# Performance work log

Measured on AMD Instinct MI355X. Metric: run time of the kernel, lower is better.

The kernel has to match this reference:

```python
import jax, jax.numpy as jnp
import numpy as np

B, S, D_IN, D_OUT = 8, 2048, 1024, 64

def setup_inputs() -> dict:
    key = jax.random.key(0)
    ks = jax.random.split(key, 6)
    return {
        "inputs_for_keys": jax.random.normal(ks[0], (B, S, D_IN), jnp.float32),
        "inputs_for_values": jax.random.normal(ks[1], (B, S, D_IN), jnp.float32),
        "inputs_for_queries": jax.random.normal(ks[2], (B, S, D_IN), jnp.float32),
        "K": jax.random.normal(ks[3], (D_IN, D_OUT), jnp.float32) * (1.0 / np.sqrt(D_IN)),
        "V": jax.random.normal(ks[4], (D_IN, D_OUT), jnp.float32) * (1.0 / np.sqrt(D_IN)),
        "Q": jax.random.normal(ks[5], (D_IN, D_OUT), jnp.float32) * (1.0 / np.sqrt(D_IN)),
    }

def reference(inputs_for_keys, inputs_for_values, inputs_for_queries, K, V, Q):
    # Project to per-head key/value/query spaces: [B, S, D_OUT]
    keys = jnp.einsum('bsd,de->bse', inputs_for_keys, K)
    values = jnp.einsum('bsd,de->bse', inputs_for_values, V)
    queries = jnp.einsum('bsd,de->bse', inputs_for_queries, Q)
    d_k = keys.shape[-1]
    # Scaled dot-product scores: [B, Sq, Sk]
    score = jnp.einsum('bqe,bke->bqk', queries, keys) / jnp.sqrt(jnp.float32(d_k))
    # Causal mask: -inf strictly above the diagonal (query i attends to keys <= i)
    sq, sk = score.shape[1], score.shape[2]
    causal = jnp.triu(jnp.full((sq, sk), -jnp.inf, dtype=score.dtype), k=1)
    score = score + causal[None, :, :]
    weights = jax.nn.softmax(score, axis=-1)
    # Attention output: [B, Sq, D_OUT]
    return jnp.einsum('bqk,bke->bqe', weights, values)
```

## Files before the change

kernel.cpp:

```cpp
#include <hip/hip_runtime.h>
#include <stdint.h>

#define BB   8
#define SS   2048
#define DIN  1024
#define DOUT 64

typedef __bf16 bf16_t;
typedef __bf16 bf16x8 __attribute__((ext_vector_type(8)));
typedef float  f32x4  __attribute__((ext_vector_type(4)));
typedef unsigned int u32x4 __attribute__((ext_vector_type(4)));

#define LOG2E 1.44269504088896f

__global__ void prep_weights(const float* __restrict__ Kw,
                             const float* __restrict__ Vw,
                             const float* __restrict__ Qw,
                             bf16_t* __restrict__ fw) {
    int proj = blockIdx.x >> 4;
    int seg  = blockIdx.x & 15;
    const float* W = (proj == 0) ? Kw : (proj == 1) ? Vw : Qw;
    float scale = (proj == 2) ? 0.125f : 1.0f;
    bf16_t* out = fw + proj * 65536;
    int base = seg * 4096;
#pragma unroll
    for (int i = 0; i < 16; ++i) {
        int idx  = base + i * 256 + threadIdx.x;
        int j    = idx & 7;
        int lane = (idx >> 3) & 63;
        int nt   = (idx >> 9) & 3;
        int kk   = idx >> 11;
        int k    = kk * 32 + (lane >> 4) * 8 + j;
        int col  = nt * 16 + (lane & 15);
        out[idx] = (bf16_t)(W[k * DOUT + col] * scale);
    }
}

__global__ __launch_bounds__(256) void proj_kernel(
    const float* __restrict__ Xk, const float* __restrict__ Xv,
    const float* __restrict__ Xq, const bf16_t* __restrict__ fw,
    bf16_t* __restrict__ outK, bf16_t* __restrict__ outV,
    bf16_t* __restrict__ outQ) {
    __shared__ __align__(16) bf16_t lds[16384];

    int proj = blockIdx.y;
    const float* X  = (proj == 0) ? Xk : (proj == 1) ? Xv : Xq;
    bf16_t* out     = (proj == 0) ? outK : (proj == 1) ? outV : outQ;
    const bf16_t* fwp = fw + proj * 65536;

    int tid  = threadIdx.x;
    int lane = tid & 63;
    int w    = tid >> 6;
    int row0 = blockIdx.x * 64 + w * 16;
    int arow = row0 + (lane & 15);
    const float* aptr = X + (size_t)arow * DIN + ((lane >> 4) * 8);

    f32x4 acc[4];
#pragma unroll
    for (int nt = 0; nt < 4; ++nt) acc[nt] = (f32x4)(0.0f);

    for (int c = 0; c < 4; ++c) {
        __syncthreads();
        const u32x4* src = (const u32x4*)(fwp + c * 16384);
        u32x4* dst = (u32x4*)lds;
#pragma unroll
        for (int i = 0; i < 8; ++i) dst[tid + 256 * i] = src[tid + 256 * i];
        __syncthreads();

#pragma unroll
        for (int kkl = 0; kkl < 8; ++kkl) {
            int kglob = c * 256 + kkl * 32;
            f32x4 a0 = *(const f32x4*)(aptr + kglob);
            f32x4 a1 = *(const f32x4*)(aptr + kglob + 4);
            bf16x8 af;
            af[0] = (bf16_t)a0[0]; af[1] = (bf16_t)a0[1];
            af[2] = (bf16_t)a0[2]; af[3] = (bf16_t)a0[3];
            af[4] = (bf16_t)a1[0]; af[5] = (bf16_t)a1[1];
            af[6] = (bf16_t)a1[2]; af[7] = (bf16_t)a1[3];
#pragma unroll
            for (int nt = 0; nt < 4; ++nt) {
                bf16x8 bfv = *(const bf16x8*)((const char*)lds +
                                ((size_t)((kkl * 4 + nt) * 64 + lane) * 16));
                acc[nt] = __builtin_amdgcn_mfma_f32_16x16x32_bf16(af, bfv, acc[nt], 0, 0, 0);
            }
        }
    }

#pragma unroll
    for (int nt = 0; nt < 4; ++nt) {
#pragma unroll
        for (int r = 0; r < 4; ++r) {
            int row = row0 + (lane >> 4) * 4 + r;
            int col = nt * 16 + (lane & 15);
            out[(size_t)row * DOUT + col] = (bf16_t)acc[nt][r];
        }
    }
}

__global__ __launch_bounds__(256) void attn_kernel(
    const bf16_t* __restrict__ Kp, const bf16_t* __restrict__ Vp,
    const bf16_t* __restrict__ Qp, float* __restrict__ out) {
    __shared__ __align__(16) bf16_t Klds[64 * 64];
    __shared__ __align__(16) bf16_t Vlds[64 * 64];
    __shared__ __align__(16) bf16_t Plds[4][16 * 64];

    int tid   = threadIdx.x;
    int lane  = tid & 63;
    int w     = tid >> 6;
    int qtile = blockIdx.x;
    int batch = blockIdx.y;

    const bf16_t* Kb = Kp + (size_t)batch * SS * DOUT;
    const bf16_t* Vb = Vp + (size_t)batch * SS * DOUT;
    const bf16_t* Qb = Qp + (size_t)batch * SS * DOUT;

    bf16x8 aq[2];
    {
        int r = qtile * 64 + w * 16 + (lane & 15);
        const bf16_t* qp = Qb + (size_t)r * DOUT + (lane >> 4) * 8;
        aq[0] = *(const bf16x8*)(qp);
        aq[1] = *(const bf16x8*)(qp + 32);
    }

    float m[4], lsum[4];
    f32x4 acc[4];
#pragma unroll
    for (int r = 0; r < 4; ++r) { m[r] = -1e30f; lsum[r] = 0.0f; }
#pragma unroll
    for (int nt = 0; nt < 4; ++nt) acc[nt] = (f32x4)(0.0f);

    int ntiles = qtile + 1;
    for (int j = 0; j < ntiles; ++j) {
        __syncthreads();
#pragma unroll
        for (int i = 0; i < 2; ++i) {
            int c   = tid + 256 * i;
            int key = c >> 3;
            int d0  = (c & 7) * 8;
            u32x4 v = *(const u32x4*)(Kb + ((size_t)(j * 64 + key)) * DOUT + d0);
            *(u32x4*)((char*)Klds + key * 128 + ((d0 * 2) ^ ((key & 7) << 4))) = v;
        }
#pragma unroll
        for (int i = 0; i < 2; ++i) {
            int c   = tid + 256 * i;
            int key = c >> 3;
            int d0  = (c & 7) * 8;
            bf16x8 v = *(const bf16x8*)(Vb + ((size_t)(j * 64 + key)) * DOUT + d0);
#pragma unroll
            for (int jj = 0; jj < 8; ++jj) {
                int d = d0 + jj;
                *(bf16_t*)((char*)Vlds + d * 128 + ((key * 2) ^ ((d & 7) << 4))) = v[jj];
            }
        }
        __syncthreads();

        f32x4 sfr[4];
#pragma unroll
        for (int nt = 0; nt < 4; ++nt) sfr[nt] = (f32x4)(0.0f);
#pragma unroll
        for (int kk = 0; kk < 2; ++kk) {
            int d0 = kk * 32 + (lane >> 4) * 8;
#pragma unroll
            for (int nt = 0; nt < 4; ++nt) {
                int key = nt * 16 + (lane & 15);
                bf16x8 bk = *(const bf16x8*)((char*)Klds + key * 128 +
                                             ((d0 * 2) ^ ((key & 7) << 4)));
                sfr[nt] = __builtin_amdgcn_mfma_f32_16x16x32_bf16(aq[kk], bk, sfr[nt], 0, 0, 0);
            }
        }

        if (j == qtile) {
#pragma unroll
            for (int nt = 0; nt < 4; ++nt) {
                int key = nt * 16 + (lane & 15);
#pragma unroll
                for (int r = 0; r < 4; ++r) {
                    int q = w * 16 + (lane >> 4) * 4 + r;
                    if (key > q) sfr[nt][r] = -1e30f;
                }
            }
        }

        float pf[4][4];
#pragma unroll
        for (int r = 0; r < 4; ++r) {
            float mx = fmaxf(fmaxf(sfr[0][r], sfr[1][r]), fmaxf(sfr[2][r], sfr[3][r]));
            mx = fmaxf(mx, __shfl_xor(mx, 1));
            mx = fmaxf(mx, __shfl_xor(mx, 2));
            mx = fmaxf(mx, __shfl_xor(mx, 4));
            mx = fmaxf(mx, __shfl_xor(mx, 8));
            float mn = fmaxf(m[r], mx);
            float scale = exp2f((m[r] - mn) * LOG2E);
            m[r] = mn;
            float rs = 0.0f;
#pragma unroll
            for (int nt = 0; nt < 4; ++nt) {
                float p = exp2f((sfr[nt][r] - mn) * LOG2E);
                pf[nt][r] = p;
                rs += p;
            }
            rs += __shfl_xor(rs, 1);
            rs += __shfl_xor(rs, 2);
            rs += __shfl_xor(rs, 4);
            rs += __shfl_xor(rs, 8);
            lsum[r] = lsum[r] * scale + rs;
#pragma unroll
            for (int nt = 0; nt < 4; ++nt) acc[nt][r] *= scale;
        }

#pragma unroll
        for (int nt = 0; nt < 4; ++nt) {
            int key = nt * 16 + (lane & 15);
#pragma unroll
            for (int r = 0; r < 4; ++r) {
                int q = (lane >> 4) * 4 + r;
                *(bf16_t*)((char*)&Plds[w][0] + q * 128 +
                           ((key * 2) ^ ((q & 7) << 4))) = (bf16_t)pf[nt][r];
            }
        }
        __syncthreads();

#pragma unroll
        for (int kk = 0; kk < 2; ++kk) {
            int k0 = kk * 32 + (lane >> 4) * 8;
            int q  = lane & 15;
            bf16x8 ap = *(const bf16x8*)((char*)&Plds[w][0] + q * 128 +
                                         ((k0 * 2) ^ ((q & 7) << 4)));
#pragma unroll
            for (int nt = 0; nt < 4; ++nt) {
                int d = nt * 16 + (lane & 15);
                bf16x8 bv = *(const bf16x8*)((char*)Vlds + d * 128 +
                                             ((k0 * 2) ^ ((d & 7) << 4)));
                acc[nt] = __builtin_amdgcn_mfma_f32_16x16x32_bf16(ap, bv, acc[nt], 0, 0, 0);
            }
        }
    }

    float* ob = out + ((size_t)batch * SS + qtile * 64 + w * 16) * DOUT;
#pragma unroll
    for (int nt = 0; nt < 4; ++nt) {
#pragma unroll
        for (int r = 0; r < 4; ++r) {
            int q = (lane >> 4) * 4 + r;
            int d = nt * 16 + (lane & 15);
            ob[(size_t)q * DOUT + d] = acc[nt][r] / lsum[r];
        }
    }
}

extern "C" void kernel_launch(void* const* d_in, const int* in_sizes, int n_in,
                              void* d_out, int out_size, void* d_ws, size_t ws_size,
                              hipStream_t stream) {
    const float* Xk = (const float*)d_in[0];
    const float* Xv = (const float*)d_in[1];
    const float* Xq = (const float*)d_in[2];
    const float* Kw = (const float*)d_in[3];
    const float* Vw = (const float*)d_in[4];
    const float* Qw = (const float*)d_in[5];

    bf16_t* Kp = (bf16_t*)d_ws;
    bf16_t* Vp = Kp + (size_t)BB * SS * DOUT;
    bf16_t* Qp = Vp + (size_t)BB * SS * DOUT;
    bf16_t* fw = Qp + (size_t)BB * SS * DOUT;

    prep_weights<<<dim3(48), dim3(256), 0, stream>>>(Kw, Vw, Qw, fw);
    proj_kernel<<<dim3(256, 3), dim3(256), 0, stream>>>(Xk, Xv, Xq, fw, Kp, Vp, Qp);
    attn_kernel<<<dim3(32, 8), dim3(256), 0, stream>>>(Kp, Vp, Qp, (float*)d_out);
}
```

Baseline: 109.5 us.

## Restructure projection kernel as split-K with LDS-staged A and register-streamed weights

The projection kernel now has each block handle 16 rows, so the grid grows from 256 to 1024 blocks per projection. Each block stages its fp32 input rows into swizzled bf16 LDS with coalesced loads. The K dimension is split across the four waves, each reading its weight fragments straight from global memory with a one-step register prefetch, and the partial results are reduced through LDS before being written out. This is meant to raise parallelism and coalescing on the memory-bound input read and to drop the repeated weight-to-LDS staging loops. In exchange it adds an LDS reduction, extra barriers and more global weight traffic per block.

```diff
diff --git a/kernel.cpp b/kernel.cpp
--- a/kernel.cpp
+++ b/kernel.cpp
@@ -7,6 +7,7 @@
 #define DOUT 64
 
 typedef __bf16 bf16_t;
+typedef __bf16 bf16x4 __attribute__((ext_vector_type(4)));
 typedef __bf16 bf16x8 __attribute__((ext_vector_type(8)));
 typedef float  f32x4  __attribute__((ext_vector_type(4)));
 typedef unsigned int u32x4 __attribute__((ext_vector_type(4)));
@@ -36,64 +37,87 @@
     }
 }
 
-__global__ __launch_bounds__(256) void proj_kernel(
+__global__ __launch_bounds__(256, 4) void proj_kernel(
     const float* __restrict__ Xk, const float* __restrict__ Xv,
     const float* __restrict__ Xq, const bf16_t* __restrict__ fw,
     bf16_t* __restrict__ outK, bf16_t* __restrict__ outV,
     bf16_t* __restrict__ outQ) {
-    __shared__ __align__(16) bf16_t lds[16384];
+    __shared__ __align__(128) char Alds[32768];
+
+    int tid  = threadIdx.x;
+    int lane = tid & 63;
+    int w    = tid >> 6;
 
     int proj = blockIdx.y;
     const float* X  = (proj == 0) ? Xk : (proj == 1) ? Xv : Xq;
     bf16_t* out     = (proj == 0) ? outK : (proj == 1) ? outV : outQ;
     const bf16_t* fwp = fw + proj * 65536;
 
-    int tid  = threadIdx.x;
-    int lane = tid & 63;
-    int w    = tid >> 6;
-    int row0 = blockIdx.x * 64 + w * 16;
-    int arow = row0 + (lane & 15);
-    const float* aptr = X + (size_t)arow * DIN + ((lane >> 4) * 8);
+    int row0 = blockIdx.x * 16;
+
+#pragma unroll
+    for (int b = 0; b < 2; ++b) {
+        f32x4 v[8];
+#pragma unroll
+        for (int j = 0; j < 8; ++j)
+            v[j] = *(const f32x4*)(X + (size_t)(row0 + b * 8 + j) * DIN + tid * 4);
+#pragma unroll
+        for (int j = 0; j < 8; ++j) {
+            int row = b * 8 + j;
+            bf16x4 bv;
+            bv[0] = (bf16_t)v[j][0]; bv[1] = (bf16_t)v[j][1];
+            bv[2] = (bf16_t)v[j][2]; bv[3] = (bf16_t)v[j][3];
+            *(bf16x4*)(Alds + row * 2048 + ((tid * 8) ^ ((row & 7) << 4))) = bv;
+        }
+    }
+    __syncthreads();
 
     f32x4 acc[4];
 #pragma unroll
     for (int nt = 0; nt < 4; ++nt) acc[nt] = (f32x4)(0.0f);
 
-    for (int c = 0; c < 4; ++c) {
-        __syncthreads();
-        const u32x4* src = (const u32x4*)(fwp + c * 16384);
-        u32x4* dst = (u32x4*)lds;
-#pragma unroll
-        for (int i = 0; i < 8; ++i) dst[tid + 256 * i] = src[tid + 256 * i];
-        __syncthreads();
-
-#pragma unroll
-        for (int kkl = 0; kkl < 8; ++kkl) {
-            int kglob = c * 256 + kkl * 32;
-            f32x4 a0 = *(const f32x4*)(aptr + kglob);
-            f32x4 a1 = *(const f32x4*)(aptr + kglob + 4);
-            bf16x8 af;
-            af[0] = (bf16_t)a0[0]; af[1] = (bf16_t)a0[1];
-            af[2] = (bf16_t)a0[2]; af[3] = (bf16_t)a0[3];
-            af[4] = (bf16_t)a1[0]; af[5] = (bf16_t)a1[1];
-            af[6] = (bf16_t)a1[2]; af[7] = (bf16_t)a1[3];
-#pragma unroll
-            for (int nt = 0; nt < 4; ++nt) {
-                bf16x8 bfv = *(const bf16x8*)((const char*)lds +
-                                ((size_t)((kkl * 4 + nt) * 64 + lane) * 16));
-                acc[nt] = __builtin_amdgcn_mfma_f32_16x16x32_bf16(af, bfv, acc[nt], 0, 0, 0);
-            }
-        }
-    }
-
-#pragma unroll
-    for (int nt = 0; nt < 4; ++nt) {
+    int arow = lane & 15;
+    const bf16_t* bq = fwp + (size_t)(w * 8) * 2048 + lane * 8;
+
+    bf16x8 bnow[4];
+#pragma unroll
+    for (int nt = 0; nt < 4; ++nt) bnow[nt] = *(const bf16x8*)(bq + nt * 512);
+
+#pragma unroll
+    for (int kkl = 0; kkl < 8; ++kkl) {
+        bf16x8 bnext[4];
+        if (kkl < 7) {
+#pragma unroll
+            for (int nt = 0; nt < 4; ++nt)
+                bnext[nt] = *(const bf16x8*)(bq + (kkl + 1) * 2048 + nt * 512);
+        }
+        int kb = (w * 256 + kkl * 32 + (lane >> 4) * 8) * 2;
+        bf16x8 a = *(const bf16x8*)(Alds + arow * 2048 + (kb ^ ((arow & 7) << 4)));
+#pragma unroll
+        for (int nt = 0; nt < 4; ++nt)
+            acc[nt] = __builtin_amdgcn_mfma_f32_16x16x32_bf16(a, bnow[nt], acc[nt], 0, 0, 0);
+#pragma unroll
+        for (int nt = 0; nt < 4; ++nt) bnow[nt] = bnext[nt];
+    }
+
+    __syncthreads();
+    float* red = (float*)Alds;
+#pragma unroll
+    for (int nt = 0; nt < 4; ++nt)
 #pragma unroll
         for (int r = 0; r < 4; ++r) {
-            int row = row0 + (lane >> 4) * 4 + r;
+            int row = (lane >> 4) * 4 + r;
             int col = nt * 16 + (lane & 15);
-            out[(size_t)row * DOUT + col] = (bf16_t)acc[nt][r];
-        }
+            red[w * 1024 + row * 64 + col] = acc[nt][r];
+        }
+    __syncthreads();
+#pragma unroll
+    for (int i = 0; i < 4; ++i) {
+        int row = (tid >> 6) * 4 + i;
+        int col = tid & 63;
+        float s = red[row * 64 + col] + red[1024 + row * 64 + col] +
+                  red[2048 + row * 64 + col] + red[3072 + row * 64 + col];
+        out[(size_t)(row0 + row) * DOUT + col] = (bf16_t)s;
     }
 }
 
@@ -264,6 +288,6 @@
     bf16_t* fw = Qp + (size_t)BB * SS * DOUT;
 
     prep_weights<<<dim3(48), dim3(256), 0, stream>>>(Kw, Vw, Qw, fw);
-    proj_kernel<<<dim3(256, 3), dim3(256), 0, stream>>>(Xk, Xv, Xq, fw, Kp, Vp, Qp);
+    proj_kernel<<<dim3(1024, 3), dim3(256), 0, stream>>>(Xk, Xv, Xq, fw, Kp, Vp, Qp);
     attn_kernel<<<dim3(32, 8), dim3(256), 0, stream>>>(Kp, Vp, Qp, (float*)d_out);
 }
```

Measured after the change: 113.0 us. 1.03x slower.

## Stage projection tiles through LDS with direct global-to-LDS loads and XOR swizzle

Applied to the files above, without the earlier changes.

The projection kernel is restructured to use 32-row tiles with 1536 blocks. The fp32 activation tile and the bf16 weight slice are streamed into LDS via global_load_lds, in 64-wide K steps, with an XOR swizzle to avoid bank conflicts. Before, each lane loaded activations directly from global memory and whole weight chunks were copied through registers. The aim is better memory-level parallelism and coalescing on the bandwidth-bound 200MB input read, at the cost of more barriers per K step and no double buffering.

```diff
diff --git a/kernel.cpp b/kernel.cpp
--- a/kernel.cpp
+++ b/kernel.cpp
@@ -7,11 +7,18 @@
 #define DOUT 64
 
 typedef __bf16 bf16_t;
+typedef __bf16 bf16x4 __attribute__((ext_vector_type(4)));
 typedef __bf16 bf16x8 __attribute__((ext_vector_type(8)));
 typedef float  f32x4  __attribute__((ext_vector_type(4)));
 typedef unsigned int u32x4 __attribute__((ext_vector_type(4)));
 
 #define LOG2E 1.44269504088896f
+
+__device__ __forceinline__ void load_lds16(const void* g, void* l) {
+    __builtin_amdgcn_global_load_lds(
+        (const __attribute__((address_space(1))) void*)g,
+        (__attribute__((address_space(3))) void*)l, 16, 0, 0);
+}
 
 __global__ void prep_weights(const float* __restrict__ Kw,
                              const float* __restrict__ Vw,
@@ -41,59 +48,60 @@
     const float* __restrict__ Xq, const bf16_t* __restrict__ fw,
     bf16_t* __restrict__ outK, bf16_t* __restrict__ outV,
     bf16_t* __restrict__ outQ) {
-    __shared__ __align__(16) bf16_t lds[16384];
+    __shared__ __align__(128) char Al[8192];
+    __shared__ __align__(128) char Bl[8192];
+
+    int tid  = threadIdx.x;
+    int lane = tid & 63;
+    int w    = tid >> 6;
 
     int proj = blockIdx.y;
     const float* X  = (proj == 0) ? Xk : (proj == 1) ? Xv : Xq;
     bf16_t* out     = (proj == 0) ? outK : (proj == 1) ? outV : outQ;
     const bf16_t* fwp = fw + proj * 65536;
 
-    int tid  = threadIdx.x;
-    int lane = tid & 63;
-    int w    = tid >> 6;
-    int row0 = blockIdx.x * 64 + w * 16;
-    int arow = row0 + (lane & 15);
-    const float* aptr = X + (size_t)arow * DIN + ((lane >> 4) * 8);
-
-    f32x4 acc[4];
-#pragma unroll
-    for (int nt = 0; nt < 4; ++nt) acc[nt] = (f32x4)(0.0f);
-
-    for (int c = 0; c < 4; ++c) {
-        __syncthreads();
-        const u32x4* src = (const u32x4*)(fwp + c * 16384);
-        u32x4* dst = (u32x4*)lds;
-#pragma unroll
-        for (int i = 0; i < 8; ++i) dst[tid + 256 * i] = src[tid + 256 * i];
-        __syncthreads();
-
-#pragma unroll
-        for (int kkl = 0; kkl < 8; ++kkl) {
-            int kglob = c * 256 + kkl * 32;
-            f32x4 a0 = *(const f32x4*)(aptr + kglob);
-            f32x4 a1 = *(const f32x4*)(aptr + kglob + 4);
+    int row0 = blockIdx.x * 32;
+
+    const float* ga = X + (size_t)(row0 + (tid >> 4)) * DIN + ((tid & 15) ^ (tid >> 4)) * 4;
+    char* alds0 = Al + (w << 10);
+    char* alds1 = Al + 4096 + (w << 10);
+    char* blds0 = Bl + (w << 10);
+    char* blds1 = Bl + 4096 + (w << 10);
+
+    f32x4 acc0 = (f32x4)(0.0f), acc1 = (f32x4)(0.0f);
+    int r   = (w & 1) * 16 + (lane & 15);
+    int nt0 = (w >> 1) * 2;
+
+    for (int kt = 0; kt < 16; ++kt) {
+        load_lds16(ga + kt * 64,               alds0);
+        load_lds16(ga + 16 * DIN + kt * 64,    alds1);
+        load_lds16(fwp + kt * 4096 + tid * 8,        blds0);
+        load_lds16(fwp + kt * 4096 + 2048 + tid * 8, blds1);
+        __syncthreads();
+
+#pragma unroll
+        for (int s = 0; s < 2; ++s) {
+            int b0 = s * 8 + (lane >> 4) * 2;
+            f32x4 lo = *(const f32x4*)(Al + r * 256 + (((b0    ) ^ (lane & 15)) << 4));
+            f32x4 hi = *(const f32x4*)(Al + r * 256 + (((b0 + 1) ^ (lane & 15)) << 4));
             bf16x8 af;
-            af[0] = (bf16_t)a0[0]; af[1] = (bf16_t)a0[1];
-            af[2] = (bf16_t)a0[2]; af[3] = (bf16_t)a0[3];
-            af[4] = (bf16_t)a1[0]; af[5] = (bf16_t)a1[1];
-            af[6] = (bf16_t)a1[2]; af[7] = (bf16_t)a1[3];
-#pragma unroll
-            for (int nt = 0; nt < 4; ++nt) {
-                bf16x8 bfv = *(const bf16x8*)((const char*)lds +
-                                ((size_t)((kkl * 4 + nt) * 64 + lane) * 16));
-                acc[nt] = __builtin_amdgcn_mfma_f32_16x16x32_bf16(af, bfv, acc[nt], 0, 0, 0);
-            }
-        }
-    }
-
-#pragma unroll
-    for (int nt = 0; nt < 4; ++nt) {
-#pragma unroll
-        for (int r = 0; r < 4; ++r) {
-            int row = row0 + (lane >> 4) * 4 + r;
-            int col = nt * 16 + (lane & 15);
-            out[(size_t)row * DOUT + col] = (bf16_t)acc[nt][r];
-        }
+            af[0] = (bf16_t)lo[0]; af[1] = (bf16_t)lo[1];
+            af[2] = (bf16_t)lo[2]; af[3] = (bf16_t)lo[3];
+            af[4] = (bf16_t)hi[0]; af[5] = (bf16_t)hi[1];
+            af[6] = (bf16_t)hi[2]; af[7] = (bf16_t)hi[3];
+            bf16x8 bf0 = *(const bf16x8*)(Bl + s * 4096 + nt0 * 1024 + lane * 16);
+            bf16x8 bf1 = *(const bf16x8*)(Bl + s * 4096 + (nt0 + 1) * 1024 + lane * 16);
+            acc0 = __builtin_amdgcn_mfma_f32_16x16x32_bf16(af, bf0, acc0, 0, 0, 0);
+            acc1 = __builtin_amdgcn_mfma_f32_16x16x32_bf16(af, bf1, acc1, 0, 0, 0);
+        }
+        __syncthreads();
+    }
+
+#pragma unroll
+    for (int j = 0; j < 4; ++j) {
+        int orow = row0 + (w & 1) * 16 + (lane >> 4) * 4 + j;
+        out[(size_t)orow * DOUT + nt0 * 16 + (lane & 15)]       = (bf16_t)acc0[j];
+        out[(size_t)orow * DOUT + (nt0 + 1) * 16 + (lane & 15)] = (bf16_t)acc1[j];
     }
 }
 
@@ -264,6 +272,6 @@
     bf16_t* fw = Qp + (size_t)BB * SS * DOUT;
 
     prep_weights<<<dim3(48), dim3(256), 0, stream>>>(Kw, Vw, Qw, fw);
-    proj_kernel<<<dim3(256, 3), dim3(256), 0, stream>>>(Xk, Xv, Xq, fw, Kp, Vp, Qp);
+    proj_kernel<<<dim3(512, 3), dim3(256), 0, stream>>>(Xk, Xv, Xq, fw, Kp, Vp, Qp);
     attn_kernel<<<dim3(32, 8), dim3(256), 0, stream>>>(Kp, Vp, Qp, (float*)d_out);
 }
```

After: 109.7 us. No clear change (+0.1%).
